# Performance work log

Measured on AMD Instinct MI355X. Metric: run time of the kernel, lower is better.

The kernel has to match this reference:

```python
import jax, jax.numpy as jnp
import numpy as np

NEG_INF = -1e30
NA_POS = 3  # position of the 'no-answer' token (after [CLS], yes, no)


def mask_pos0(x, mask):
    # keep x where mask==1, set to large negative where mask==0
    return x * mask + (1.0 - mask) * NEG_INF


def make_span_mask(seq_len, max_ans_len):
    m = jnp.tril(jnp.triu(jnp.ones((seq_len, seq_len), jnp.float32), 0), max_ans_len - 1)
    m = m.at[:4, :].set(0.0)
    m = m.at[1, 1].set(1.0)
    m = m.at[2, 2].set(1.0)
    m = m.at[NA_POS, NA_POS].set(1.0)
    return m


def setup_inputs() -> dict:
    key = jax.random.key(0)
    k1, k2, k3 = jax.random.split(key, 3)
    B, S, H = 8, 4096, 1024
    seq_hiddens = jax.random.normal(k1, (B, S, H), jnp.float32)
    ans_mask = jnp.ones((B, S), jnp.float32)
    W_qa = jax.random.normal(k2, (H, 2), jnp.float32) * (1.0 / np.sqrt(H))
    b_qa = jnp.zeros((2,), jnp.float32)
    return {"seq_hiddens": seq_hiddens, "ans_mask": ans_mask, "W_qa": W_qa,
            "b_qa": b_qa, "top_k": 5}


def reference(seq_hiddens, ans_mask, W_qa, b_qa, top_k):
    B, S, H = seq_hiddens.shape
    max_ans_len = 30
    # linear QA head: (B,S,H) @ (H,2) -> (B,S,2)
    span_logits = jnp.einsum('bsh,hc->bsc', seq_hiddens, W_qa) + b_qa
    masked_span_logits = mask_pos0(span_logits, ans_mask[:, :, None])
    start_logits = masked_span_logits[..., 0]  # (B,S)
    end_logits = masked_span_logits[..., 1]    # (B,S)
    # outer-sum span scores: (B,S,S)
    span_scores = start_logits[:, :, None] + end_logits[:, None, :]
    span_mask = make_span_mask(S, max_ans_len)[None]
    masked_span_scores = mask_pos0(span_scores, span_mask)
    flat = masked_span_scores.reshape(B, S * S)
    _, top_span = jax.lax.top_k(flat, top_k)  # (B,k)
    top_start = top_span // S
    top_end = top_span % S
    return start_logits, end_logits, top_start, top_end
```

## Files before the change

### kernel.cpp

```cpp
#include <hip/hip_runtime.h>
#include <cfloat>

#define NEG_INF_F (-1e30f)

constexpr int BB = 8, SS = 4096, HH = 1024;
constexpr int TOTAL = BB * SS;
constexpr int MAXLEN = 30;
constexpr int RPB = 256;
constexpr int BLK_PER_B = SS / RPB;
constexpr int TK_GRID = BB * BLK_PER_B;

__global__ __launch_bounds__(256) void qa_logits_kernel(
    const float* __restrict__ X,
    const float* __restrict__ mask,
    const float* __restrict__ W,
    const float* __restrict__ bqa,
    float* __restrict__ out,
    unsigned* __restrict__ cnt) {
  if (blockIdx.x == 0 && threadIdx.x < BB) cnt[threadIdx.x] = 0u;
  int row  = (int)((blockIdx.x * (size_t)blockDim.x + threadIdx.x) >> 6);
  int lane = threadIdx.x & 63;
  if (row >= TOTAL) return;
  const float* rp = X + (size_t)row * HH;
  float s0 = 0.f, s1 = 0.f;
#pragma unroll
  for (int k = 0; k < HH / 256; ++k) {
    int h = (k * 64 + lane) * 4;
    const float4 x   = *reinterpret_cast<const float4*>(rp + h);
    const float4 w01 = *reinterpret_cast<const float4*>(W + 2 * h);
    const float4 w23 = *reinterpret_cast<const float4*>(W + 2 * h + 4);
    s0 += x.x * w01.x + x.y * w01.z + x.z * w23.x + x.w * w23.z;
    s1 += x.x * w01.y + x.y * w01.w + x.z * w23.y + x.w * w23.w;
  }
#pragma unroll
  for (int off = 32; off > 0; off >>= 1) {
    s0 += __shfl_down(s0, off);
    s1 += __shfl_down(s1, off);
  }
  if (lane == 0) {
    float m = mask[row];
    float inv = 1.f - m;
    out[row]         = (s0 + bqa[0]) * m + inv * NEG_INF_F;
    out[TOTAL + row] = (s1 + bqa[1]) * m + inv * NEG_INF_F;
  }
}

__device__ __forceinline__ unsigned long long pack_key(float v, unsigned idx) {
  unsigned u = __float_as_uint(v);
  u = (u & 0x80000000u) ? ~u : (u | 0x80000000u);
  return ((unsigned long long)u << 32) | (unsigned long long)(0xFFFFFFFFu - idx);
}

__device__ __forceinline__ void k5_insert(unsigned long long k[5], unsigned long long nk) {
  if (nk <= k[4]) return;
  k[4] = nk;
  unsigned long long t;
  if (k[4] > k[3]) { t = k[3]; k[3] = k[4]; k[4] = t; }
  if (k[3] > k[2]) { t = k[2]; k[2] = k[3]; k[3] = t; }
  if (k[2] > k[1]) { t = k[1]; k[1] = k[2]; k[2] = t; }
  if (k[1] > k[0]) { t = k[0]; k[0] = k[1]; k[1] = t; }
}

__device__ __forceinline__ void wave_top5_u64(unsigned long long k[5],
                                              unsigned long long r[5]) {
#pragma unroll
  for (int q = 0; q < 5; ++q) {
    unsigned long long m = k[0];
    if (k[1] > m) m = k[1];
    if (k[2] > m) m = k[2];
    if (k[3] > m) m = k[3];
    if (k[4] > m) m = k[4];
#pragma unroll
    for (int off = 1; off < 64; off <<= 1) {
      unsigned long long o = __shfl_xor(m, off);
      if (o > m) m = o;
    }
    r[q] = m;
#pragma unroll
    for (int p = 0; p < 5; ++p)
      if (k[p] == m) k[p] = 0ull;
  }
}

__global__ __launch_bounds__(RPB) void topk_kernel(
    const float* __restrict__ logits,
    float* __restrict__ out,
    unsigned long long* __restrict__ ws,
    unsigned* __restrict__ cnt) {
  const int b  = blockIdx.x / BLK_PER_B;
  const int rb = blockIdx.x % BLK_PER_B;
  const int i0 = rb * RPB;
  const int t  = (int)threadIdx.x;
  const int lane = t & 63;
  const int w = t >> 6;

  __shared__ float s_st[RPB];
  __shared__ float s_en[RPB + 32];
  __shared__ unsigned long long sk[(RPB / 64) * 5];

  const float* st = logits + (size_t)b * SS + i0;
  const float* en = logits + (size_t)(BB + b) * SS + i0;
  const int n_en = min(SS - i0, RPB + MAXLEN - 1);

  if (t < RPB / 4)
    *reinterpret_cast<float4*>(&s_st[t * 4]) =
        *reinterpret_cast<const float4*>(st + t * 4);
  else if (t >= 64 && t < 64 + (n_en + 3) / 4) {
    int r = t - 64;
    if (r * 4 + 4 <= n_en)
      *reinterpret_cast<float4*>(&s_en[r * 4]) =
          *reinterpret_cast<const float4*>(en + r * 4);
    else
      for (int c = r * 4; c < n_en; ++c) s_en[c] = en[c];
  }
  __syncthreads();

  unsigned long long k5[5] = {0, 0, 0, 0, 0};
  const int i = i0 + t;
  if (i >= 4) {
    float sv = s_st[t];
    unsigned base = (unsigned)(i * SS + i);
    int cap = n_en - t;
#pragma unroll
    for (int c = 0; c < MAXLEN; ++c)
      if (c < cap) k5_insert(k5, pack_key(sv + s_en[t + c], base + c));
  } else if (i >= 1) {
    k5_insert(k5, pack_key(s_st[t] + s_en[t], (unsigned)(i * SS + i)));
  }

  unsigned long long r5[5];
  wave_top5_u64(k5, r5);
  if (lane == 0) {
#pragma unroll
    for (int q = 0; q < 5; ++q) sk[w * 5 + q] = r5[q];
  }
  __syncthreads();

  if (w == 0) {
    unsigned long long m5[5] = {0, 0, 0, 0, 0};
    if (lane < (RPB / 64) * 5) m5[0] = sk[lane];
    unsigned long long f5[5];
    wave_top5_u64(m5, f5);

    unsigned old = 0;
    if (lane == 0) {
#pragma unroll
      for (int q = 0; q < 5; ++q)
        __hip_atomic_store(&ws[blockIdx.x * 5 + q], f5[q],
                           __ATOMIC_RELAXED, __HIP_MEMORY_SCOPE_AGENT);
      __threadfence();
      old = __hip_atomic_fetch_add(&cnt[b], 1u, __ATOMIC_RELAXED,
                                   __HIP_MEMORY_SCOPE_AGENT);
    }
    old = __shfl(old, 0);

    if (old == (unsigned)(BLK_PER_B - 1)) {
      __threadfence();
      const unsigned long long* src = ws + (size_t)b * BLK_PER_B * 5;
      unsigned long long g5[5] = {0, 0, 0, 0, 0};
      g5[0] = __hip_atomic_load(&src[lane], __ATOMIC_RELAXED,
                                __HIP_MEMORY_SCOPE_AGENT);
      if (lane < BLK_PER_B * 5 - 64)
        g5[1] = __hip_atomic_load(&src[64 + lane], __ATOMIC_RELAXED,
                                  __HIP_MEMORY_SCOPE_AGENT);
      unsigned long long h5[5];
      wave_top5_u64(g5, h5);
      if (lane == 0) {
        float* ts = out + 2 * (size_t)TOTAL;
        float* te = ts + BB * 5;
#pragma unroll
        for (int q = 0; q < 5; ++q) {
          unsigned idx = 0xFFFFFFFFu - (unsigned)(h5[q] & 0xFFFFFFFFull);
          ts[b * 5 + q] = (float)(idx >> 12);
          te[b * 5 + q] = (float)(idx & (SS - 1));
        }
      }
    }
  }
}

extern "C" void kernel_launch(void* const* d_in, const int* in_sizes, int n_in,
                              void* d_out, int out_size, void* d_ws, size_t ws_size,
                              hipStream_t stream) {
  const float* X    = (const float*)d_in[0];
  const float* mask = (const float*)d_in[1];
  const float* W    = (const float*)d_in[2];
  const float* bqa  = (const float*)d_in[3];
  float* out = (float*)d_out;

  unsigned long long* ws = (unsigned long long*)d_ws;
  unsigned* cnt = (unsigned*)((char*)d_ws + TK_GRID * 5 * sizeof(unsigned long long));

  qa_logits_kernel<<<TOTAL / 4, 256, 0, stream>>>(X, mask, W, bqa, out, cnt);
  topk_kernel<<<TK_GRID, RPB, 0, stream>>>(out, out, ws, cnt);
}
```

Before: 37.65 us.

## Split each span row across two threads and drop shared-memory staging in top-k

The top-k kernel now runs 1024-thread blocks covering 512 start rows each. Two threads share a row, each scoring 15 end candidates. End logits are read straight from global memory into registers, replacing the cooperative shared-memory staging and its barrier. Block-level and cross-block reductions are resized for 16 waves and 8 blocks per batch. This shortens the serial insertion chain per thread, at the cost of redundant global loads and only 64 blocks in the grid.

```diff
diff --git a/kernel.cpp b/kernel.cpp
--- a/kernel.cpp
+++ b/kernel.cpp
@@ -6,8 +6,10 @@
 constexpr int BB = 8, SS = 4096, HH = 1024;
 constexpr int TOTAL = BB * SS;
 constexpr int MAXLEN = 30;
-constexpr int RPB = 256;
-constexpr int BLK_PER_B = SS / RPB;
+constexpr int TK_TPB = 1024;
+constexpr int TK_RPB = 512;
+constexpr int CPT = 15;
+constexpr int BLK_PER_B = SS / TK_RPB;
 constexpr int TK_GRID = BB * BLK_PER_B;
 
 __global__ __launch_bounds__(256) void qa_logits_kernel(
@@ -82,50 +84,42 @@
   }
 }
 
-__global__ __launch_bounds__(RPB) void topk_kernel(
+__global__ __launch_bounds__(TK_TPB) void topk_kernel(
     const float* __restrict__ logits,
     float* __restrict__ out,
     unsigned long long* __restrict__ ws,
     unsigned* __restrict__ cnt) {
-  const int b  = blockIdx.x / BLK_PER_B;
-  const int rb = blockIdx.x % BLK_PER_B;
-  const int i0 = rb * RPB;
-  const int t  = (int)threadIdx.x;
+  const int t = (int)threadIdx.x;
   const int lane = t & 63;
   const int w = t >> 6;
+  const int b  = blockIdx.x >> 3;
+  const int rb = blockIdx.x & 7;
+  const int lr = t >> 1;
+  const int sub = t & 1;
+  const int i = rb * TK_RPB + lr;
 
-  __shared__ float s_st[RPB];
-  __shared__ float s_en[RPB + 32];
-  __shared__ unsigned long long sk[(RPB / 64) * 5];
+  const float* st = logits + (size_t)b * SS;
+  const float* en = logits + (size_t)(BB + b) * SS;
 
-  const float* st = logits + (size_t)b * SS + i0;
-  const float* en = logits + (size_t)(BB + b) * SS + i0;
-  const int n_en = min(SS - i0, RPB + MAXLEN - 1);
-
-  if (t < RPB / 4)
-    *reinterpret_cast<float4*>(&s_st[t * 4]) =
-        *reinterpret_cast<const float4*>(st + t * 4);
-  else if (t >= 64 && t < 64 + (n_en + 3) / 4) {
-    int r = t - 64;
-    if (r * 4 + 4 <= n_en)
-      *reinterpret_cast<float4*>(&s_en[r * 4]) =
-          *reinterpret_cast<const float4*>(en + r * 4);
-    else
-      for (int c = r * 4; c < n_en; ++c) s_en[c] = en[c];
-  }
-  __syncthreads();
+  __shared__ unsigned long long sk[(TK_TPB / 64) * 5];
 
   unsigned long long k5[5] = {0, 0, 0, 0, 0};
-  const int i = i0 + t;
+  const float sv = st[i];
+
   if (i >= 4) {
-    float sv = s_st[t];
-    unsigned base = (unsigned)(i * SS + i);
-    int cap = n_en - t;
+    const int c0 = sub * CPT;
+    float e[CPT];
 #pragma unroll
-    for (int c = 0; c < MAXLEN; ++c)
-      if (c < cap) k5_insert(k5, pack_key(sv + s_en[t + c], base + c));
-  } else if (i >= 1) {
-    k5_insert(k5, pack_key(s_st[t] + s_en[t], (unsigned)(i * SS + i)));
+    for (int c = 0; c < CPT; ++c) {
+      int j = i + c0 + c;
+      float v = en[j];
+      e[c] = (j < SS) ? v : NEG_INF_F;
+    }
+    unsigned base = (unsigned)(i * SS + i + c0);
+#pragma unroll
+    for (int c = 0; c < CPT; ++c) k5_insert(k5, pack_key(sv + e[c], base + c));
+  } else if (i >= 1 && sub == 0) {
+    k5_insert(k5, pack_key(sv + en[i], (unsigned)(i * SS + i)));
   }
 
   unsigned long long r5[5];
@@ -138,7 +132,8 @@
 
   if (w == 0) {
     unsigned long long m5[5] = {0, 0, 0, 0, 0};
-    if (lane < (RPB / 64) * 5) m5[0] = sk[lane];
+    m5[0] = sk[lane];
+    if (lane < (TK_TPB / 64) * 5 - 64) m5[1] = sk[64 + lane];
     unsigned long long f5[5];
     wave_top5_u64(m5, f5);
 
@@ -158,10 +153,8 @@
       __threadfence();
       const unsigned long long* src = ws + (size_t)b * BLK_PER_B * 5;
       unsigned long long g5[5] = {0, 0, 0, 0, 0};
-      g5[0] = __hip_atomic_load(&src[lane], __ATOMIC_RELAXED,
-                                __HIP_MEMORY_SCOPE_AGENT);
-      if (lane < BLK_PER_B * 5 - 64)
-        g5[1] = __hip_atomic_load(&src[64 + lane], __ATOMIC_RELAXED,
+      if (lane < BLK_PER_B * 5)
+        g5[0] = __hip_atomic_load(&src[lane], __ATOMIC_RELAXED,
                                   __HIP_MEMORY_SCOPE_AGENT);
       unsigned long long h5[5];
       wave_top5_u64(g5, h5);
@@ -192,5 +185,5 @@
   unsigned* cnt = (unsigned*)((char*)d_ws + TK_GRID * 5 * sizeof(unsigned long long));
 
   qa_logits_kernel<<<TOTAL / 4, 256, 0, stream>>>(X, mask, W, bqa, out, cnt);
-  topk_kernel<<<TK_GRID, RPB, 0, stream>>>(out, out, ws, cnt);
+  topk_kernel<<<TK_GRID, TK_TPB, 0, stream>>>(out, out, ws, cnt);
 }
```

Result: faster. 36.53 us (-3.0%).
